# Performance work log

Measured on AMD Instinct MI355X. Metric: run time of the kernel, lower is better.

The kernel has to match this reference:

```python
import jax, jax.numpy as jnp
import numpy as np
from jax import lax

# ---- static config (from cfg) ----
B, NCLS, CREG, H, W = 16, 3, 50, 96, 320
K = 100                  # DETECTIONS_PER_IMG
DOWN = 4                 # BACKBONE.DOWN_RATIO
THRESH = 0.2             # DETECTIONS_THRESHOLD
IMG_W, IMG_H = W * DOWN, H * DOWN
EPS = 1e-6
# channel layout in pred_reg (kvper):
#  0:4 dim_2d | 4:6 offset_3d | 6:9 dim_3d | 9:25 orient | 25:45 corner_offset
#  45:48 corner_uncertainty | 48 depth | 49 depth_uncertainty


def setup_inputs() -> dict:
    key = jax.random.key(0)
    k1, k2, k3 = jax.random.split(key, 3)
    # shift heatmap logits negative so only a sparse set passes the threshold
    pred_hmp = jax.random.normal(k1, (B, NCLS, H, W), jnp.float32) * 2.0 - 2.0
    pred_reg = jax.random.normal(k2, (B, CREG, H, W), jnp.float32) * 0.5
    # KITTI P2 intrinsics: [f_u, c_u, f_v, c_v] per image
    calib = jnp.tile(jnp.array([[721.5377, 609.5593, 721.5377, 172.854]],
                               jnp.float32), (B, 1))
    pad_size = jnp.zeros((B, 2), jnp.float32)
    # per-class mean dims (l, h, w): Car / Pedestrian / Cyclist
    dim_mean = jnp.array([[3.88, 1.53, 1.63],
                          [0.84, 1.76, 0.66],
                          [1.76, 1.73, 0.60]], jnp.float32)
    return {"pred_hmp": pred_hmp, "pred_reg": pred_reg, "calib": calib,
            "pad_size": pad_size, "dim_mean": dim_mean}


def reference(pred_hmp, pred_reg, calib, pad_size, dim_mean):
    f32 = pred_hmp.dtype
    # ---- nms_hm: sigmoid + 3x3 max-pool suppression ----
    heat = jax.nn.sigmoid(pred_hmp)
    hmax = lax.reduce_window(heat, -jnp.inf, lax.max,
                             (1, 1, 3, 3), (1, 1, 1, 1), 'SAME')
    heat = jnp.where(hmax == heat, heat, jnp.zeros((), f32))
    # ---- select_topk (CenterNet-style): per-class topk then global topk ----
    flat = heat.reshape(B, NCLS, H * W)
    s1, i1 = lax.top_k(flat, K)                        # (B, C, K)
    s2, i2 = lax.top_k(s1.reshape(B, NCLS * K), K)     # (B, K)
    classes = i2 // K                                  # (B, K)
    inds = jnp.take_along_axis(i1.reshape(B, NCLS * K), i2, axis=1)  # flat h*w idx
    ys = (inds // W).astype(f32)
    xs = (inds % W).astype(f32)
    # ---- select_point_of_interest: gather 50-ch reg features at topk points ----
    regf = pred_reg.transpose(0, 2, 3, 1).reshape(B, H * W, CREG)
    pois = jnp.take_along_axis(regf, inds[:, :, None], axis=1).reshape(B * K, CREG)

    scores = s2.reshape(-1)                            # (N,) N = B*K
    cls = classes.reshape(-1)
    pts = jnp.stack([xs.reshape(-1), ys.reshape(-1)], axis=1)  # (N, 2)
    mask = (scores >= THRESH).astype(f32)
    bidx = jnp.repeat(jnp.arange(B), K)                # per-detection batch index

    reg2d = jax.nn.relu(pois[:, 0:4])                  # l, t, r, b
    off3d = pois[:, 4:6]
    dimoff = pois[:, 6:9]
    kpt = pois[:, 25:45].reshape(-1, 10, 2)            # 10 keypoints (x, y)
    cunc = jnp.exp(pois[:, 45:48])                     # corner uncertainty
    doff = pois[:, 48]
    dunc = jnp.exp(pois[:, 49:50])                     # direct depth uncertainty

    # ---- decode_dim3d: exp offset scaled by class mean dims ----
    dims = jnp.exp(dimoff) * dim_mean[cls]             # (N, 3); dims[:,1] = height
    h3d = dims[:, 1]

    # ---- decode_depth (inv_sigmoid) ----
    direct_depth = jnp.clip(1.0 / jax.nn.sigmoid(doff) - 1.0, 0.1, 100.0)

    # ---- decode_depth_from_kpts_batch: pinhole height -> depth ----
    fu = calib[bidx, 0]; cu = calib[bidx, 1]
    fv = calib[bidx, 2]; cv = calib[bidx, 3]
    ctr_h = kpt[:, 8, 1] - kpt[:, 9, 1]                       # bottom - top center
    c02_h = kpt[:, jnp.array([0, 2]), 1] - kpt[:, jnp.array([4, 6]), 1]
    c13_h = kpt[:, jnp.array([1, 3]), 1] - kpt[:, jnp.array([5, 7]), 1]
    d_ctr = fu * h3d / (jax.nn.relu(ctr_h) * DOWN + EPS)
    d_02 = ((fu * h3d)[:, None] / (jax.nn.relu(c02_h) * DOWN + EPS)).mean(axis=1)
    d_13 = ((fu * h3d)[:, None] / (jax.nn.relu(c13_h) * DOWN + EPS)).mean(axis=1)
    kpt_depths = jnp.clip(jnp.stack([d_ctr, d_02, d_13], axis=1), 0.1, 100.0)

    # ---- 'soft' depth ensemble: uncertainty-weighted average ----
    comb_d = jnp.concatenate([direct_depth[:, None], kpt_depths], axis=1)  # (N,4)
    comb_u = jnp.concatenate([dunc, cunc], axis=1)                          # (N,4)
    wts = 1.0 / comb_u
    wts = wts / wts.sum(axis=1, keepdims=True)
    depth = (comb_d * wts).sum(axis=1)
    depth_err = (wts * comb_u).sum(axis=1)

    # ---- decode_box2d_fcos ----
    pad = pad_size[bidx]                               # (N, 2)
    box2d = jnp.concatenate([pts - reg2d[:, :2], pts + reg2d[:, 2:]],
                            axis=1) * DOWN - jnp.tile(pad, (1, 2))
    hi = jnp.array([IMG_W - 1, IMG_H - 1, IMG_W - 1, IMG_H - 1], f32)
    box2d = jnp.clip(box2d, 0.0, hi)

    # ---- decode_loc3d: unproject projected 3D center at estimated depth ----
    proj = (pts + off3d) * DOWN - pad                  # (N, 2) image-plane uv
    x3 = (proj[:, 0] - cu) * depth / fu
    y3 = (proj[:, 1] - cv) * depth / fv
    loc3d = jnp.stack([x3, y3, depth], axis=1)

    result = jnp.concatenate([cls.astype(f32)[:, None], scores[:, None],
                              box2d, dims, loc3d, depth_err[:, None]], axis=1)
    return result * mask[:, None]                      # (B*K, 13)
```

## Files before the change

kernel.cpp:

```cpp
#include <hip/hip_runtime.h>
#include <math.h>


#define W_ 320
#define H_ 96
#define HW_ (W_ * H_)
#define LDSW 322
#define LDSH 98
#define CANDCAP 4096
#define BITS_02 0x3E4CCCCDu
#define FLAG_MAGIC 0x5EC0DE01

__global__ __launch_bounds__(1024) void monoflex_all(
    const float* __restrict__ hmp,
    const float* __restrict__ reg,
    const float* __restrict__ calib,
    const float* __restrict__ pad_size,
    const float* __restrict__ dim_mean,
    float* __restrict__ out,
    unsigned long long* __restrict__ s1,
    int* __restrict__ flags) {
  const int plane = blockIdx.x;
  const int b = plane / 3;
  const int cls0 = plane - b * 3;
  const int t = threadIdx.x;
  const int lane = t & 63;
  const float* p = hmp + (size_t)plane * HW_;

  __shared__ __align__(16) float lp[LDSH * LDSW];
  __shared__ unsigned cand[CANDCAP];
  __shared__ unsigned long long skey[1024];
  __shared__ int hist[1024];
  __shared__ int cnt, mcnt, cutbin;

  if (t == 0) { cnt = 0; mcnt = 0; cutbin = 0; }
  hist[t] = 0;

  if (t < 836) {
    int idx;
    if (t < 322)      idx = t;
    else if (t < 644) idx = 97 * LDSW + (t - 322);
    else if (t < 740) idx = (t - 644 + 1) * LDSW;
    else              idx = (t - 740 + 1) * LDSW + 321;
    lp[idx] = -INFINITY;
  }

  for (int i = t; i < HW_; i += 1024) {
    float v = p[i];
    int r = i / W_;
    int col = i - r * W_;
    lp[(r + 1) * LDSW + col + 1] = v;
  }
  __syncthreads();

  for (int i = t; i < HW_; i += 1024) {
    int r = i / W_;
    int c = i - r * W_;
    int cc = c + 1;
    float a = lp[r * LDSW + cc];
    float v = lp[(r + 1) * LDSW + cc];
    float e = lp[(r + 2) * LDSW + cc];
    float vm = fmaxf(fmaxf(a, v), e);
    float vmL = __shfl_up(vm, 1);
    float vmR = __shfl_down(vm, 1);
    if (lane == 0)
      vmL = fmaxf(fmaxf(lp[r * LDSW + cc - 1], lp[(r + 1) * LDSW + cc - 1]),
                  lp[(r + 2) * LDSW + cc - 1]);
    if (lane == 63)
      vmR = fmaxf(fmaxf(lp[r * LDSW + cc + 1], lp[(r + 1) * LDSW + cc + 1]),
                  lp[(r + 2) * LDSW + cc + 1]);
    float m9 = fmaxf(fmaxf(vmL, vm), vmR);
    bool pass = (v >= m9);
    if (pass) {
      float s = 1.0f / (1.0f + expf(-v));
      pass = (s >= 0.2f);
      if (pass) {
        unsigned bits = __float_as_uint(s);
        unsigned bin = (bits - BITS_02) >> 15;
        if (bin > 1023u) bin = 1023u;
        atomicAdd(&hist[bin], 1);
      }
    }
    unsigned long long act = __ballot(pass);
    if (pass) {
      int rank = __popcll(act & ((1ull << lane) - 1));
      int base;
      if (rank == 0) base = atomicAdd(&cnt, (int)__popcll(act));
      base = __shfl(base, (int)__ffsll(act) - 1);
      int q = base + rank;
      if (q < CANDCAP) cand[q] = (unsigned)i;
    }
  }
  __syncthreads();

  if (t < 64) {
    int ssum = 0;
    #pragma unroll
    for (int k2 = 0; k2 < 16; ++k2) ssum += hist[t * 16 + k2];
    int suf = ssum;
    #pragma unroll
    for (int off = 1; off < 64; off <<= 1) {
      int o = __shfl_down(suf, off);
      if (lane + off < 64) suf += o;
    }
    int sufn = __shfl_down(suf, 1);
    if (lane == 63) sufn = 0;
    if (suf >= 100 && sufn < 100) {
      int acc = sufn;
      int cb = t * 16;
      for (int k2 = t * 16 + 15; k2 >= t * 16; --k2) {
        acc += hist[k2];
        if (acc >= 100) { cb = k2; break; }
      }
      cutbin = cb;
    }
  }
  __syncthreads();
  const int cb = cutbin;
  const int n = min(cnt, CANDCAP);

  for (int i = t; i < n; i += 1024) {
    unsigned gi = cand[i];
    int row = (int)gi / W_;
    int col = (int)gi - row * W_;
    float v = lp[(row + 1) * LDSW + col + 1];
    float s = 1.0f / (1.0f + expf(-v));
    unsigned bits = __float_as_uint(s);
    unsigned bin = (bits - BITS_02) >> 15;
    if (bin > 1023u) bin = 1023u;
    if ((int)bin >= cb) {
      int q = atomicAdd(&mcnt, 1);
      if (q < 1024)
        skey[q] = ((unsigned long long)bits << 32) |
                  (unsigned long long)(0xFFFFFFFFu - gi);
    }
  }
  __syncthreads();
  const int m = min(mcnt, 1024);
  const int N = (m <= 128) ? 128 : ((m <= 256) ? 256 : 1024);
  if (t < N && t >= m) skey[t] = 0ULL;
  __syncthreads();

  for (int k = 2; k <= N; k <<= 1) {
    for (int j = k >> 1; j > 0; j >>= 1) {
      if (t < N) {
        int l = t ^ j;
        if (l > t) {
          unsigned long long a = skey[t], b2 = skey[l];
          if ((a > b2) == ((t & k) != 0)) { skey[t] = b2; skey[l] = a; }
        }
      }
      __syncthreads();
    }
  }

  if (t < 100) s1[plane * 100 + t] = skey[t];
  __threadfence();
  __syncthreads();
  if (t == 0) atomicExch(&flags[plane], FLAG_MAGIC);
  if (cls0 != 0) return;

  unsigned long long* topk = (unsigned long long*)lp;
  int*   selgi  = (int*)(lp + 600);
  int*   selcls = (int*)(lp + 700);
  float* selsc  = (float*)(lp + 800);
  float* pbuf   = lp + 900;

  if (t < 100) topk[t] = skey[t];
  if (t == 0)
    while (atomicCAS(&flags[plane + 1], FLAG_MAGIC, FLAG_MAGIC) != FLAG_MAGIC) {}
  if (t == 64)
    while (atomicCAS(&flags[plane + 2], FLAG_MAGIC, FLAG_MAGIC) != FLAG_MAGIC) {}
  __syncthreads();
  if (t >= 100 && t < 300) topk[t] = atomicAdd(&s1[b * 300 + t], 0ULL);
  __syncthreads();

  if (t < 300) {
    int c2 = t / 100, r2 = t - c2 * 100;
    unsigned long long key = topk[t];
    unsigned bits = (unsigned)(key >> 32);
    int rank = r2;
    #pragma unroll
    for (int cp = 0; cp < 3; ++cp) {
      if (cp == c2) continue;
      const unsigned long long* L = topk + cp * 100;
      int lo = 0, hi = 100;
      while (lo < hi) {
        int mid = (lo + hi) >> 1;
        if ((unsigned)(L[mid] >> 32) > bits) lo = mid + 1; else hi = mid;
      }
      int cntGT = lo;
      if (cp < c2) {
        lo = cntGT; hi = 100;
        while (lo < hi) {
          int mid = (lo + hi) >> 1;
          if ((unsigned)(L[mid] >> 32) >= bits) lo = mid + 1; else hi = mid;
        }
        rank += lo;
      } else {
        rank += cntGT;
      }
    }
    if (rank < 100) {
      bool valid = (bits != 0u);
      selgi[rank]  = valid ? (int)(0xFFFFFFFFu - (unsigned)(key & 0xFFFFFFFFull))
                           : -1;
      selcls[rank] = c2;
      selsc[rank]  = __uint_as_float(bits);
    }
  }
  __syncthreads();

  const float* rbase = reg + (size_t)b * 50 * HW_;
  {
    float gv[5];
    int gx[5];
    #pragma unroll
    for (int rr = 0; rr < 5; ++rr) {
      int idx = rr * 1024 + t;
      bool ok = idx < 5000;
      int row = ok ? (idx % 100) : 0;
      int ch  = ok ? (idx / 100) : 0;
      int gi = selgi[row];
      gv[rr] = (ok && gi >= 0) ? rbase[(size_t)ch * HW_ + gi] : 0.0f;
      gx[rr] = row * 51 + ch;
    }
    #pragma unroll
    for (int rr = 0; rr < 5; ++rr) {
      int idx = rr * 1024 + t;
      if (idx < 5000) pbuf[gx[rr]] = gv[rr];
    }
  }
  __syncthreads();

  if (t < 100) {
    float* orow = out + ((size_t)b * 100 + t) * 13;
    int gi = selgi[t];
    if (gi < 0) {
      #pragma unroll
      for (int i = 0; i < 13; ++i) orow[i] = 0.0f;
    } else {
      const float* pp = &pbuf[t * 51];
      int cls = selcls[t];
      float score = selsc[t];
      int yy = gi / W_;
      int xx = gi - yy * W_;
      float x = (float)xx, y = (float)yy;

      float fu = calib[b * 4 + 0], cu = calib[b * 4 + 1];
      float fv = calib[b * 4 + 2], cv = calib[b * 4 + 3];
      float pad0 = pad_size[b * 2 + 0], pad1 = pad_size[b * 2 + 1];

      float r0 = fmaxf(pp[0], 0.f), r1 = fmaxf(pp[1], 0.f);
      float r2 = fmaxf(pp[2], 0.f), r3 = fmaxf(pp[3], 0.f);
      float bx0 = fminf(fmaxf((x - r0) * 4.f - pad0, 0.f), 1279.f);
      float by0 = fminf(fmaxf((y - r1) * 4.f - pad1, 0.f), 383.f);
      float bx1 = fminf(fmaxf((x + r2) * 4.f - pad0, 0.f), 1279.f);
      float by1 = fminf(fmaxf((y + r3) * 4.f - pad1, 0.f), 383.f);

      float d0 = expf(pp[6]) * dim_mean[cls * 3 + 0];
      float d1 = expf(pp[7]) * dim_mean[cls * 3 + 1];
      float d2 = expf(pp[8]) * dim_mean[cls * 3 + 2];
      float h3d = d1;

      float sig = 1.0f / (1.0f + expf(-pp[48]));
      float ddepth = fminf(fmaxf(1.0f / sig - 1.0f, 0.1f), 100.0f);

      float fh = fu * h3d;
      float d_ctr = fh / (fmaxf(pp[42] - pp[44], 0.f) * 4.f + 1e-6f);
      float d02 = 0.5f * (fh / (fmaxf(pp[26] - pp[34], 0.f) * 4.f + 1e-6f) +
                          fh / (fmaxf(pp[30] - pp[38], 0.f) * 4.f + 1e-6f));
      float d13 = 0.5f * (fh / (fmaxf(pp[28] - pp[36], 0.f) * 4.f + 1e-6f) +
                          fh / (fmaxf(pp[32] - pp[40], 0.f) * 4.f + 1e-6f));
      float kd0 = fminf(fmaxf(d_ctr, 0.1f), 100.f);
      float kd1 = fminf(fmaxf(d02, 0.1f), 100.f);
      float kd2 = fminf(fmaxf(d13, 0.1f), 100.f);

      float u0 = expf(pp[49]), u1 = expf(pp[45]);
      float u2 = expf(pp[46]), u3 = expf(pp[47]);
      float w0 = 1.f / u0, w1 = 1.f / u1, w2 = 1.f / u2, w3 = 1.f / u3;
      float S = w0 + w1 + w2 + w3;
      float depth = (ddepth * w0 + kd0 * w1 + kd1 * w2 + kd2 * w3) / S;
      float derr = (w0 * u0 + w1 * u1 + w2 * u2 + w3 * u3) / S;

      float px = (x + pp[4]) * 4.f - pad0;
      float py = (y + pp[5]) * 4.f - pad1;
      float x3 = (px - cu) * depth / fu;
      float y3 = (py - cv) * depth / fv;

      orow[0] = (float)cls;
      orow[1] = score;
      orow[2] = bx0; orow[3] = by0; orow[4] = bx1; orow[5] = by1;
      orow[6] = d0;  orow[7] = d1;  orow[8] = d2;
      orow[9] = x3;  orow[10] = y3; orow[11] = depth;
      orow[12] = derr;
    }
  }
}

extern "C" void kernel_launch(void* const* d_in, const int* in_sizes, int n_in,
                              void* d_out, int out_size, void* d_ws, size_t ws_size,
                              hipStream_t stream) {
  const float* hmp   = (const float*)d_in[0];
  const float* reg   = (const float*)d_in[1];
  const float* calib = (const float*)d_in[2];
  const float* pads  = (const float*)d_in[3];
  const float* dm    = (const float*)d_in[4];
  float* out = (float*)d_out;

  unsigned long long* s1 = (unsigned long long*)d_ws;
  int* flags = (int*)((char*)d_ws + 48 * 100 * 8);

  monoflex_all<<<dim3(48), dim3(1024), 0, stream>>>(hmp, reg, calib, pads, dm,
                                                    out, s1, flags);
}
```

Baseline: 184.3 us.

## Split each heatmap plane across two blocks and merge half top-k lists

Each class plane is now processed by two blocks, one per half of the rows, giving 96 blocks instead of 48. The 3x3 max is computed straight from global memory instead of being staged in a padded LDS tile. Candidates store their sigmoid key at once so the second pass skips recomputation, and small candidate sets are sorted in registers with a single-wave shuffle bitonic sort. A leader block per image waits on five flags and merges the half lists per class before the global merge. The aim is more parallelism across CUs and less LDS traffic and barriers, at the cost of redundant global loads and more inter-block spin-waiting.

```diff
diff --git a/kernel.cpp b/kernel.cpp
--- a/kernel.cpp
+++ b/kernel.cpp
@@ -5,11 +5,16 @@
 #define W_ 320
 #define H_ 96
 #define HW_ (W_ * H_)
-#define LDSW 322
-#define LDSH 98
-#define CANDCAP 4096
+#define CANDCAP 2048
+#define SKEYCAP 512
 #define BITS_02 0x3E4CCCCDu
 #define FLAG_MAGIC 0x5EC0DE01
+
+__device__ inline unsigned long long shflx64(unsigned long long v, int m) {
+  int lo = __shfl_xor((int)(unsigned)v, m, 64);
+  int hi = __shfl_xor((int)(unsigned)(v >> 32), m, 64);
+  return ((unsigned long long)(unsigned)hi << 32) | (unsigned)lo;
+}
 
 __global__ __launch_bounds__(1024) void monoflex_all(
     const float* __restrict__ hmp,
@@ -20,62 +25,66 @@
     float* __restrict__ out,
     unsigned long long* __restrict__ s1,
     int* __restrict__ flags) {
-  const int plane = blockIdx.x;
-  const int b = plane / 3;
-  const int cls0 = plane - b * 3;
+  const int ph = blockIdx.x;
+  const int half = ph & 1;
+  const int plane = ph >> 1;
   const int t = threadIdx.x;
   const int lane = t & 63;
   const float* p = hmp + (size_t)plane * HW_;
-
-  __shared__ __align__(16) float lp[LDSH * LDSW];
-  __shared__ unsigned cand[CANDCAP];
-  __shared__ unsigned long long skey[1024];
+  const int r0 = half * 48;
+
+  __shared__ unsigned long long cand[CANDCAP];
+  __shared__ unsigned long long skey[SKEYCAP];
   __shared__ int hist[1024];
   __shared__ int cnt, mcnt, cutbin;
+  __shared__ unsigned long long halfkeys[600];
+  __shared__ unsigned long long classlist[300];
+  __shared__ int selgi[100];
+  __shared__ int selcls[100];
+  __shared__ float selsc[100];
+  __shared__ float pbuf[100 * 51];
 
   if (t == 0) { cnt = 0; mcnt = 0; cutbin = 0; }
   hist[t] = 0;
-
-  if (t < 836) {
-    int idx;
-    if (t < 322)      idx = t;
-    else if (t < 644) idx = 97 * LDSW + (t - 322);
-    else if (t < 740) idx = (t - 644 + 1) * LDSW;
-    else              idx = (t - 740 + 1) * LDSW + 321;
-    lp[idx] = -INFINITY;
-  }
-
-  for (int i = t; i < HW_; i += 1024) {
-    float v = p[i];
-    int r = i / W_;
-    int col = i - r * W_;
-    lp[(r + 1) * LDSW + col + 1] = v;
-  }
-  __syncthreads();
-
-  for (int i = t; i < HW_; i += 1024) {
-    int r = i / W_;
-    int c = i - r * W_;
-    int cc = c + 1;
-    float a = lp[r * LDSW + cc];
-    float v = lp[(r + 1) * LDSW + cc];
-    float e = lp[(r + 2) * LDSW + cc];
-    float vm = fmaxf(fmaxf(a, v), e);
+  __syncthreads();
+
+  for (int idx = t; idx < 48 * W_; idx += 1024) {
+    int rr = idx / W_;
+    int c = idx - rr * W_;
+    int r = r0 + rr;
+    int g = r * W_ + c;
+    float v = p[g];
+    float up = (r > 0) ? p[g - W_] : -INFINITY;
+    float dn = (r < 95) ? p[g + W_] : -INFINITY;
+    float vm = fmaxf(fmaxf(up, dn), v);
     float vmL = __shfl_up(vm, 1);
     float vmR = __shfl_down(vm, 1);
-    if (lane == 0)
-      vmL = fmaxf(fmaxf(lp[r * LDSW + cc - 1], lp[(r + 1) * LDSW + cc - 1]),
-                  lp[(r + 2) * LDSW + cc - 1]);
-    if (lane == 63)
-      vmR = fmaxf(fmaxf(lp[r * LDSW + cc + 1], lp[(r + 1) * LDSW + cc + 1]),
-                  lp[(r + 2) * LDSW + cc + 1]);
-    float m9 = fmaxf(fmaxf(vmL, vm), vmR);
-    bool pass = (v >= m9);
+    if (lane == 0) {
+      vmL = -INFINITY;
+      if (c > 0) {
+        float lv = p[g - 1];
+        float lu = (r > 0) ? p[g - W_ - 1] : -INFINITY;
+        float ld = (r < 95) ? p[g + W_ - 1] : -INFINITY;
+        vmL = fmaxf(fmaxf(lu, ld), lv);
+      }
+    }
+    if (lane == 63) {
+      vmR = -INFINITY;
+      if (c < 319) {
+        float rv = p[g + 1];
+        float ru = (r > 0) ? p[g - W_ + 1] : -INFINITY;
+        float rd = (r < 95) ? p[g + W_ + 1] : -INFINITY;
+        vmR = fmaxf(fmaxf(ru, rd), rv);
+      }
+    }
+    float m9 = fmaxf(fmaxf(vmL, vmR), vm);
+    bool pass = (v >= m9) && (v > -1.3865f);
+    unsigned bits = 0u;
     if (pass) {
       float s = 1.0f / (1.0f + expf(-v));
       pass = (s >= 0.2f);
       if (pass) {
-        unsigned bits = __float_as_uint(s);
+        bits = __float_as_uint(s);
         unsigned bin = (bits - BITS_02) >> 15;
         if (bin > 1023u) bin = 1023u;
         atomicAdd(&hist[bin], 1);
@@ -88,7 +97,9 @@
       if (rank == 0) base = atomicAdd(&cnt, (int)__popcll(act));
       base = __shfl(base, (int)__ffsll(act) - 1);
       int q = base + rank;
-      if (q < CANDCAP) cand[q] = (unsigned)i;
+      if (q < CANDCAP)
+        cand[q] = ((unsigned long long)bits << 32) |
+                  (unsigned long long)(0xFFFFFFFFu - (unsigned)g);
     }
   }
   __syncthreads();
@@ -120,70 +131,106 @@
   const int n = min(cnt, CANDCAP);
 
   for (int i = t; i < n; i += 1024) {
-    unsigned gi = cand[i];
-    int row = (int)gi / W_;
-    int col = (int)gi - row * W_;
-    float v = lp[(row + 1) * LDSW + col + 1];
-    float s = 1.0f / (1.0f + expf(-v));
-    unsigned bits = __float_as_uint(s);
-    unsigned bin = (bits - BITS_02) >> 15;
+    unsigned long long k = cand[i];
+    unsigned bin = ((unsigned)(k >> 32) - BITS_02) >> 15;
     if (bin > 1023u) bin = 1023u;
     if ((int)bin >= cb) {
       int q = atomicAdd(&mcnt, 1);
-      if (q < 1024)
-        skey[q] = ((unsigned long long)bits << 32) |
-                  (unsigned long long)(0xFFFFFFFFu - gi);
-    }
-  }
-  __syncthreads();
-  const int m = min(mcnt, 1024);
-  const int N = (m <= 128) ? 128 : ((m <= 256) ? 256 : 1024);
-  if (t < N && t >= m) skey[t] = 0ULL;
-  __syncthreads();
-
-  for (int k = 2; k <= N; k <<= 1) {
-    for (int j = k >> 1; j > 0; j >>= 1) {
-      if (t < N) {
-        int l = t ^ j;
-        if (l > t) {
-          unsigned long long a = skey[t], b2 = skey[l];
-          if ((a > b2) == ((t & k) != 0)) { skey[t] = b2; skey[l] = a; }
+      if (q < SKEYCAP) skey[q] = k;
+    }
+  }
+  __syncthreads();
+  const int m = min(mcnt, SKEYCAP);
+  if (t >= m && t < SKEYCAP) skey[t] = 0ULL;
+  __syncthreads();
+
+  unsigned long long* dst = s1 + (size_t)ph * 100;
+  if (m <= 128) {
+    if (t < 64) {
+      unsigned long long e0 = skey[lane], e1 = skey[64 + lane];
+      #pragma unroll
+      for (int k = 2; k <= 128; k <<= 1) {
+        #pragma unroll
+        for (int j = k >> 1; j > 0; j >>= 1) {
+          if (j == 64) {
+            if (e0 <= e1) { unsigned long long tmp = e0; e0 = e1; e1 = tmp; }
+          } else {
+            bool lower = ((lane & j) == 0);
+            {
+              unsigned long long o = shflx64(e0, j);
+              bool asc = ((lane & k) != 0);
+              unsigned long long lv = lower ? e0 : o, uv = lower ? o : e0;
+              if ((lv > uv) == asc) e0 = o;
+            }
+            {
+              unsigned long long o = shflx64(e1, j);
+              bool asc = (((64 + lane) & k) != 0);
+              unsigned long long lv = lower ? e1 : o, uv = lower ? o : e1;
+              if ((lv > uv) == asc) e1 = o;
+            }
+          }
         }
       }
-      __syncthreads();
-    }
-  }
-
-  if (t < 100) s1[plane * 100 + t] = skey[t];
-  __threadfence();
-  __syncthreads();
-  if (t == 0) atomicExch(&flags[plane], FLAG_MAGIC);
-  if (cls0 != 0) return;
-
-  unsigned long long* topk = (unsigned long long*)lp;
-  int*   selgi  = (int*)(lp + 600);
-  int*   selcls = (int*)(lp + 700);
-  float* selsc  = (float*)(lp + 800);
-  float* pbuf   = lp + 900;
-
-  if (t < 100) topk[t] = skey[t];
-  if (t == 0)
-    while (atomicCAS(&flags[plane + 1], FLAG_MAGIC, FLAG_MAGIC) != FLAG_MAGIC) {}
-  if (t == 64)
-    while (atomicCAS(&flags[plane + 2], FLAG_MAGIC, FLAG_MAGIC) != FLAG_MAGIC) {}
-  __syncthreads();
-  if (t >= 100 && t < 300) topk[t] = atomicAdd(&s1[b * 300 + t], 0ULL);
+      dst[lane] = e0;
+      if (lane < 36) dst[64 + lane] = e1;
+      __threadfence();
+      if (lane == 0) atomicExch(&flags[ph], FLAG_MAGIC);
+    }
+  } else {
+    const int N = (m <= 256) ? 256 : 512;
+    for (int k = 2; k <= N; k <<= 1) {
+      for (int j = k >> 1; j > 0; j >>= 1) {
+        if (t < N) {
+          int l = t ^ j;
+          if (l > t) {
+            unsigned long long a = skey[t], b2 = skey[l];
+            if ((a > b2) == ((t & k) != 0)) { skey[t] = b2; skey[l] = a; }
+          }
+        }
+        __syncthreads();
+      }
+    }
+    if (t < 100) dst[t] = skey[t];
+    __threadfence();
+    __syncthreads();
+    if (t == 0) atomicExch(&flags[ph], FLAG_MAGIC);
+  }
+
+  if ((ph % 6) != 0) return;
+
+  const int b = ph / 6;
+  if (t < 5)
+    while (atomicCAS(&flags[ph + 1 + t], FLAG_MAGIC, FLAG_MAGIC) != FLAG_MAGIC) {}
+  __syncthreads();
+  if (t < 600) halfkeys[t] = atomicAdd(&s1[b * 600 + t], 0ULL);
+  if (t < 300) classlist[t] = 0ULL;
+  __syncthreads();
+
+  if (t < 600) {
+    int c2 = t / 200, h = (t / 100) & 1, r = t % 100;
+    unsigned long long key = halfkeys[t];
+    if (key != 0ULL) {
+      const unsigned long long* L = &halfkeys[(c2 * 2 + (1 - h)) * 100];
+      int lo = 0, hi = 100;
+      while (lo < hi) {
+        int mid = (lo + hi) >> 1;
+        if (L[mid] > key) lo = mid + 1; else hi = mid;
+      }
+      int cr = r + lo;
+      if (cr < 100) classlist[c2 * 100 + cr] = key;
+    }
+  }
   __syncthreads();
 
   if (t < 300) {
     int c2 = t / 100, r2 = t - c2 * 100;
-    unsigned long long key = topk[t];
+    unsigned long long key = classlist[t];
     unsigned bits = (unsigned)(key >> 32);
     int rank = r2;
     #pragma unroll
     for (int cp = 0; cp < 3; ++cp) {
       if (cp == c2) continue;
-      const unsigned long long* L = topk + cp * 100;
+      const unsigned long long* L = classlist + cp * 100;
       int lo = 0, hi = 100;
       while (lo < hi) {
         int mid = (lo + hi) >> 1;
@@ -216,19 +263,19 @@
     float gv[5];
     int gx[5];
     #pragma unroll
-    for (int rr = 0; rr < 5; ++rr) {
-      int idx = rr * 1024 + t;
+    for (int rr2 = 0; rr2 < 5; ++rr2) {
+      int idx = rr2 * 1024 + t;
       bool ok = idx < 5000;
       int row = ok ? (idx % 100) : 0;
       int ch  = ok ? (idx / 100) : 0;
       int gi = selgi[row];
-      gv[rr] = (ok && gi >= 0) ? rbase[(size_t)ch * HW_ + gi] : 0.0f;
-      gx[rr] = row * 51 + ch;
-    }
-    #pragma unroll
-    for (int rr = 0; rr < 5; ++rr) {
-      int idx = rr * 1024 + t;
-      if (idx < 5000) pbuf[gx[rr]] = gv[rr];
+      gv[rr2] = (ok && gi >= 0) ? rbase[(size_t)ch * HW_ + gi] : 0.0f;
+      gx[rr2] = row * 51 + ch;
+    }
+    #pragma unroll
+    for (int rr2 = 0; rr2 < 5; ++rr2) {
+      int idx = rr2 * 1024 + t;
+      if (idx < 5000) pbuf[gx[rr2]] = gv[rr2];
     }
   }
   __syncthreads();
@@ -251,12 +298,12 @@
       float fv = calib[b * 4 + 2], cv = calib[b * 4 + 3];
       float pad0 = pad_size[b * 2 + 0], pad1 = pad_size[b * 2 + 1];
 
-      float r0 = fmaxf(pp[0], 0.f), r1 = fmaxf(pp[1], 0.f);
-      float r2 = fmaxf(pp[2], 0.f), r3 = fmaxf(pp[3], 0.f);
-      float bx0 = fminf(fmaxf((x - r0) * 4.f - pad0, 0.f), 1279.f);
-      float by0 = fminf(fmaxf((y - r1) * 4.f - pad1, 0.f), 383.f);
-      float bx1 = fminf(fmaxf((x + r2) * 4.f - pad0, 0.f), 1279.f);
-      float by1 = fminf(fmaxf((y + r3) * 4.f - pad1, 0.f), 383.f);
+      float rA = fmaxf(pp[0], 0.f), rB = fmaxf(pp[1], 0.f);
+      float rC = fmaxf(pp[2], 0.f), rD = fmaxf(pp[3], 0.f);
+      float bx0 = fminf(fmaxf((x - rA) * 4.f - pad0, 0.f), 1279.f);
+      float by0 = fminf(fmaxf((y - rB) * 4.f - pad1, 0.f), 383.f);
+      float bx1 = fminf(fmaxf((x + rC) * 4.f - pad0, 0.f), 1279.f);
+      float by1 = fminf(fmaxf((y + rD) * 4.f - pad1, 0.f), 383.f);
 
       float d0 = expf(pp[6]) * dim_mean[cls * 3 + 0];
       float d1 = expf(pp[7]) * dim_mean[cls * 3 + 1];
@@ -309,8 +356,8 @@
   float* out = (float*)d_out;
 
   unsigned long long* s1 = (unsigned long long*)d_ws;
-  int* flags = (int*)((char*)d_ws + 48 * 100 * 8);
-
-  monoflex_all<<<dim3(48), dim3(1024), 0, stream>>>(hmp, reg, calib, pads, dm,
+  int* flags = (int*)((char*)d_ws + 96 * 100 * 8);
+
+  monoflex_all<<<dim3(96), dim3(1024), 0, stream>>>(hmp, reg, calib, pads, dm,
                                                     out, s1, flags);
 }
```

Result: faster. 173.0 us (-6.1%).
